# Kernel tuning notes

Measured on AMD Instinct MI355X. Metric: run time of the kernel, lower is better.

## Reference

```python
import jax, jax.numpy as jnp
import numpy as np
import math

SENT_DIM = 1024
HIDDEN_DIM = 1024
NUM_HEADS = 8
ALIGN_DIM = HIDDEN_DIM // NUM_HEADS  # 128
N_SENT = 4096
N_KNOW = 4096


def setup_inputs() -> dict:
    key = jax.random.key(0)
    ks = jax.random.split(key, 12)
    sentences = jax.random.normal(ks[0], (N_SENT, SENT_DIM), dtype=jnp.float32)
    knowledge = jax.random.normal(ks[1], (N_KNOW, SENT_DIM), dtype=jnp.float32)
    # binary multiplicative mask over knowledge entries, broadcast over sentence rows
    mask = (jax.random.uniform(ks[2], (N_KNOW,)) > 0.5).astype(jnp.float32)
    lim_p = 1.0 / math.sqrt(SENT_DIM)
    # per-head projections, stacked: [H, sent_dim, align_dim]
    Ws = jax.random.uniform(ks[3], (NUM_HEADS, SENT_DIM, ALIGN_DIM), minval=-lim_p, maxval=lim_p)
    bs = jax.random.uniform(ks[4], (NUM_HEADS, ALIGN_DIM), minval=-lim_p, maxval=lim_p)
    Wk = jax.random.uniform(ks[5], (NUM_HEADS, SENT_DIM, ALIGN_DIM), minval=-lim_p, maxval=lim_p)
    bk = jax.random.uniform(ks[6], (NUM_HEADS, ALIGN_DIM), minval=-lim_p, maxval=lim_p)
    # transform MLP: Linear(H*sent_dim -> sent_dim), ReLU, (dropout=identity in eval), Linear(sent_dim -> sent_dim)
    lim1 = 1.0 / math.sqrt(NUM_HEADS * SENT_DIM)
    W1 = jax.random.uniform(ks[7], (NUM_HEADS * SENT_DIM, SENT_DIM), minval=-lim1, maxval=lim1)
    b1 = jax.random.uniform(ks[8], (SENT_DIM,), minval=-lim1, maxval=lim1)
    lim2 = 1.0 / math.sqrt(SENT_DIM)
    W2 = jax.random.uniform(ks[9], (SENT_DIM, SENT_DIM), minval=-lim2, maxval=lim2)
    b2 = jax.random.uniform(ks[10], (SENT_DIM,), minval=-lim2, maxval=lim2)
    return {"sentences": sentences, "knowledge": knowledge, "mask": mask,
            "Ws": Ws, "bs": bs, "Wk": Wk, "bk": bk,
            "W1": W1, "b1": b1, "W2": W2, "b2": b2}


def reference(sentences, knowledge, mask, Ws, bs, Wk, bk, W1, b1, W2, b2):
    # Batched over heads (original loops in Python over heads)
    S = jnp.einsum('nd,hde->hne', sentences, Ws) + bs[:, None, :]   # [H, Ns, A]
    K = jnp.einsum('md,hde->hme', knowledge, Wk) + bk[:, None, :]   # [H, Nk, A]
    scores = jnp.einsum('hne,hme->hnm', S, K) / jnp.sqrt(jnp.float32(ALIGN_DIM))
    attn = jax.nn.softmax(scores, axis=-1)                          # softmax over knowledge dim
    attn = attn * mask[None, None, :]                               # post-softmax multiplicative mask
    head_out = jnp.einsum('hnm,md->hnd', attn, knowledge)           # [H, Ns, sent_dim]
    # concat heads along feature dim: [Ns, H*sent_dim]
    concat = jnp.transpose(head_out, (1, 0, 2)).reshape(head_out.shape[1], -1)
    h = jax.nn.relu(concat @ W1 + b1)                               # dropout identity in eval
    output = h @ W2 + b2                                            # [Ns, sent_dim]
    # weights cat along dim 0: [H*Ns, Nk]
    weights = attn.reshape(-1, attn.shape[-1])
    return output, weights
```

## Files before the change

### kernel.cpp

```cpp
#include <hip/hip_runtime.h>
#include <hip/hip_bf16.h>

typedef __attribute__((ext_vector_type(4))) float  floatx4;
typedef __attribute__((ext_vector_type(8))) short  shortx8;
typedef __attribute__((ext_vector_type(4))) short  shortx4;

__device__ __forceinline__ short f2bf(float x) {
    union { float f; unsigned u; } v; v.f = x;
    unsigned r = v.u + 0x7FFFu + ((v.u >> 16) & 1u);
    return (short)(r >> 16);
}
__device__ __forceinline__ float bf2f(short x) {
    union { unsigned u; float f; } c; c.u = ((unsigned)(unsigned short)x) << 16;
    return c.f;
}
__device__ __forceinline__ short f2bf_hw(float x) {
    union { __hip_bfloat16 h; short s; } u;
    u.h = __float2bfloat16(x);
    return u.s;
}

__device__ __forceinline__ void gload16(const void* g, void* l) {
    __builtin_amdgcn_global_load_lds(
        (const __attribute__((address_space(1))) void*)g,
        (__attribute__((address_space(3))) void*)l, 16, 0, 0);
}


__global__ void cast_bf16(const float* __restrict__ src, short* __restrict__ dst, int n4) {
    int i = blockIdx.x * blockDim.x + threadIdx.x;
    if (i < n4) {
        floatx4 v = ((const floatx4*)src)[i];
        shortx4 s;
        s[0] = f2bf(v[0]); s[1] = f2bf(v[1]); s[2] = f2bf(v[2]); s[3] = f2bf(v[3]);
        ((shortx4*)dst)[i] = s;
    }
}

__global__ void transpose_cast(const float* __restrict__ src, short* __restrict__ dst,
                               int R, int C, long szSrc, long szDst) {
    __shared__ float tile[32][33];
    const float* s = src + (long)blockIdx.z * szSrc;
    short* d = dst + (long)blockIdx.z * szDst;
    int c0 = blockIdx.x * 32, r0 = blockIdx.y * 32;
    for (int i = threadIdx.y; i < 32; i += 8)
        tile[i][threadIdx.x] = s[(long)(r0 + i) * C + c0 + threadIdx.x];
    __syncthreads();
    for (int i = threadIdx.y; i < 32; i += 8)
        d[(long)(c0 + i) * R + r0 + threadIdx.x] = f2bf(tile[threadIdx.x][i]);
}


#define BM 128
#define BN 128
#define BK 32

template<bool AF32, bool RELU, bool CF32, bool XSWZ>
__global__ __launch_bounds__(256) void gemm_nt(
    const void* __restrict__ Ap, const short* __restrict__ Bp, void* __restrict__ Cp,
    const float* __restrict__ bias, float alpha,
    int K, int lda, int ldb, int ldc,
    long sAz, long sBz, long sCz, long aHX, long sbias)
{
    __shared__ __align__(16) char  AsB[AF32 ? BM * BK * 4 : BM * BK * 2];
    __shared__ __align__(16) short Bs[BN * BK];
    short* AsS = reinterpret_cast<short*>(AsB);
    float* AsF = reinterpret_cast<float*>(AsB);

    int bx, by, bz;
    if constexpr (XSWZ) {
        int id = blockIdx.x + (blockIdx.y << 3) + (blockIdx.z << 8);
        bx = (id >> 3) & 7;
        int g = (id & 7) | ((id >> 6) << 3);
        by = g & 31; bz = g >> 5;
    } else { bx = blockIdx.x; by = blockIdx.y; bz = blockIdx.z; }

    const int t    = threadIdx.x;
    const int m0   = by * BM;
    const int n0   = bx * BN;
    const int z    = bz;
    const int wave = t >> 6, lane = t & 63;
    const int wm   = (wave & 1) * 64, wn = (wave >> 1) * 64;
    const int quad = lane >> 4, l16 = lane & 15;
    const int wofs = t & ~63;

    const short* Bz = Bp + (long)z * sBz;

    const int srow = t >> 2;
    const int ssw  = ((t & 3) ^ ((t >> 3) & 3)) * 8;
    const short* bSrc = Bz + (long)(n0 + srow) * ldb + ssw;

    const short* aSrc  = nullptr;
    const float* aSrcF = nullptr;
    if constexpr (AF32) {
        const float* Az = (const float*)Ap + (long)z * sAz;
        aSrcF = Az + (long)(m0 + (t >> 3)) * lda + (((t & 7) ^ ((t >> 3) & 7)) * 4);
    } else {
        const short* Az = (const short*)Ap + (long)z * sAz;
        aSrc = Az + (long)(m0 + srow) * lda + ssw;
    }

    const int ra = wm + l16, rb = wn + l16;
    const int sa = (quad ^ ((ra >> 1) & 3)) * 8;
    const int sb = (quad ^ ((rb >> 1) & 3)) * 8;
    const int s0 = (((quad << 1)    ) ^ (ra & 7)) * 4;
    const int s1 = (((quad << 1) | 1) ^ (ra & 7)) * 4;

    floatx4 acc[4][4] = {};

    for (int k0 = 0; k0 < K; k0 += BK) {
        const long off = (long)k0 + (long)(k0 >> 12) * aHX;
        __syncthreads();
        if constexpr (AF32) {
            #pragma unroll
            for (int p = 0; p < 4; ++p)
                gload16(aSrcF + (long)p * 32 * lda + off,
                        AsF + (p * 256 + wofs) * 4);
        } else {
            gload16(aSrc + off,                  AsS + wofs * 8);
            gload16(aSrc + (long)64 * lda + off, AsS + (256 + wofs) * 8);
        }
        gload16(bSrc + k0,                  &Bs[wofs * 8]);
        gload16(bSrc + (long)64 * ldb + k0, &Bs[(256 + wofs) * 8]);
        __syncthreads();

        shortx8 af[4], bfr[4];
        #pragma unroll
        for (int i = 0; i < 4; ++i) {
            if constexpr (AF32) {
                const float* pf = AsF + (ra + 16 * i) * 32;
                floatx4 f0 = *(const floatx4*)(pf + s0);
                floatx4 f1 = *(const floatx4*)(pf + s1);
                shortx8 s;
                s[0] = f2bf_hw(f0[0]); s[1] = f2bf_hw(f0[1]);
                s[2] = f2bf_hw(f0[2]); s[3] = f2bf_hw(f0[3]);
                s[4] = f2bf_hw(f1[0]); s[5] = f2bf_hw(f1[1]);
                s[6] = f2bf_hw(f1[2]); s[7] = f2bf_hw(f1[3]);
                af[i] = s;
            } else {
                af[i] = *(const shortx8*)(AsS + (ra + 16 * i) * 32 + sa);
            }
        }
        #pragma unroll
        for (int j = 0; j < 4; ++j)
            bfr[j] = *(const shortx8*)(&Bs[(rb + 16 * j) * 32 + sb]);
        #pragma unroll
        for (int i = 0; i < 4; ++i)
            #pragma unroll
            for (int j = 0; j < 4; ++j)
                acc[i][j] = __builtin_amdgcn_mfma_f32_16x16x32_bf16(af[i], bfr[j], acc[i][j], 0, 0, 0);
    }

    float bv[4];
    #pragma unroll
    for (int j = 0; j < 4; ++j)
        bv[j] = bias ? (bias + (long)z * sbias)[n0 + wn + j * 16 + l16] : 0.0f;

    #pragma unroll
    for (int i = 0; i < 4; ++i) {
        #pragma unroll
        for (int e = 0; e < 4; ++e) {
            long row = m0 + wm + i * 16 + quad * 4 + e;
            #pragma unroll
            for (int j = 0; j < 4; ++j) {
                float val = acc[i][j][e] * alpha + bv[j];
                if (RELU) val = fmaxf(val, 0.0f);
                long col = n0 + wn + j * 16 + l16;
                if (CF32) ((float*)Cp + (long)z * sCz)[row * ldc + col] = val;
                else      ((short*)Cp + (long)z * sCz)[row * ldc + col] = f2bf(val);
            }
        }
    }
}


__global__ __launch_bounds__(256) void softmax_mask(float* __restrict__ attn,
                                                    const float* __restrict__ mask) {
    float* p = attn + (long)blockIdx.x * 4096;
    const int t = threadIdx.x;
    float v[16];
    float mx = -3.4e38f;
    #pragma unroll
    for (int i = 0; i < 16; ++i) { v[i] = p[t + 256 * i]; mx = fmaxf(mx, v[i]); }
    #pragma unroll
    for (int o = 32; o > 0; o >>= 1) mx = fmaxf(mx, __shfl_down(mx, o));
    __shared__ float r1[4], r2[4];
    const int lane = t & 63, w = t >> 6;
    if (lane == 0) r1[w] = mx;
    __syncthreads();
    mx = fmaxf(fmaxf(r1[0], r1[1]), fmaxf(r1[2], r1[3]));
    float s = 0.f;
    #pragma unroll
    for (int i = 0; i < 16; ++i) { v[i] = __expf(v[i] - mx); s += v[i]; }
    #pragma unroll
    for (int o = 32; o > 0; o >>= 1) s += __shfl_down(s, o);
    if (lane == 0) r2[w] = s;
    __syncthreads();
    s = r2[0] + r2[1] + r2[2] + r2[3];
    const float inv = 1.0f / s;
    #pragma unroll
    for (int i = 0; i < 16; ++i) p[t + 256 * i] = v[i] * inv * mask[t + 256 * i];
}


__global__ __launch_bounds__(256) void reduce_heads(const short* __restrict__ part,
                                                    const float* __restrict__ b1,
                                                    short* __restrict__ h_bf) {
    int i = blockIdx.x * blockDim.x + threadIdx.x;
    float s[8] = {0,0,0,0,0,0,0,0};
    #pragma unroll
    for (int z = 0; z < 4; ++z) {
        shortx8 v = ((const shortx8*)(part + (long)z * 4194304))[i];
        #pragma unroll
        for (int e = 0; e < 8; ++e) s[e] += bf2f(v[e]);
    }
    int j0 = (i * 8) & 1023;
    shortx8 o;
    #pragma unroll
    for (int e = 0; e < 8; ++e) o[e] = f2bf(fmaxf(s[e] + b1[j0 + e], 0.f));
    ((shortx8*)h_bf)[i] = o;
}


extern "C" void kernel_launch(void* const* d_in, const int* in_sizes, int n_in,
                              void* d_out, int out_size, void* d_ws, size_t ws_size,
                              hipStream_t stream) {
    const float* sentences = (const float*)d_in[0];
    const float* knowledge = (const float*)d_in[1];
    const float* mask      = (const float*)d_in[2];
    const float* Ws        = (const float*)d_in[3];
    const float* bs        = (const float*)d_in[4];
    const float* Wk        = (const float*)d_in[5];
    const float* bk        = (const float*)d_in[6];
    const float* W1        = (const float*)d_in[7];
    const float* b1        = (const float*)d_in[8];
    const float* W2        = (const float*)d_in[9];
    const float* b2        = (const float*)d_in[10];

    float* out  = (float*)d_out;
    float* attn = out + 4194304;

    char* ws = (char*)d_ws;
    short* V_T     = (short*)(ws);
    short* W2T     = (short*)(ws + 67108864);
    short* h_bf    = (short*)(ws + 69206016);
    float* bias2   = (float*)(ws + 77594624);
    short* sent_bf = (short*)(ws + 77611008);
    short* know_bf = (short*)(ws + 85999616);
    short* WsT     = (short*)(ws + 94388224);
    short* WkT     = (short*)(ws + 96485376);
    short* W1T     = (short*)(ws + 98582528);
    short* S_bf    = (short*)(ws + 115359744);
    short* K_bf    = (short*)(ws + 123748352);
    short* part    = (short*)(ws + 77611008);
    (void)K_bf;

    cast_bf16<<<4096, 256, 0, stream>>>(sentences, sent_bf, 1048576);
    cast_bf16<<<4096, 256, 0, stream>>>(knowledge, know_bf, 1048576);
    transpose_cast<<<dim3(4, 32, 8),  dim3(32, 8), 0, stream>>>(Ws, WsT, 1024, 128, 131072, 131072);
    transpose_cast<<<dim3(4, 32, 8),  dim3(32, 8), 0, stream>>>(Wk, WkT, 1024, 128, 131072, 131072);
    transpose_cast<<<dim3(32, 32, 8), dim3(32, 8), 0, stream>>>(W1, W1T, 1024, 1024, 1048576, 1048576);
    transpose_cast<<<dim3(32, 32, 1), dim3(32, 8), 0, stream>>>(W2, W2T, 1024, 1024, 0, 0);
    hipMemcpyAsync(bias2,        bs, 4096, hipMemcpyDeviceToDevice, stream);
    hipMemcpyAsync(bias2 + 1024, bk, 4096, hipMemcpyDeviceToDevice, stream);

    gemm_nt<false, false, false, false><<<dim3(8, 32, 2), 256, 0, stream>>>(
        sent_bf, WsT, S_bf, bias2, 1.0f, 1024, 1024, 1024, 1024,
        4194304, 1048576, 4194304, 0, 1024);
    gemm_nt<false, false, false, false><<<dim3(32, 8, 8), 256, 0, stream>>>(
        W1T, know_bf, V_T, nullptr, 1.0f, 1024, 1024, 1024, 32768,
        1048576, 0, 4096, 0, 0);
    gemm_nt<false, false, true, false><<<dim3(32, 32, 8), 256, 0, stream>>>(
        S_bf, K_bf, attn, nullptr, 0.08838834764831845f, 128, 1024, 1024, 4096,
        128, 128, 16777216, 0, 0);
    softmax_mask<<<32768, 256, 0, stream>>>(attn, mask);
    gemm_nt<true, false, false, true><<<dim3(8, 32, 4), 256, 0, stream>>>(
        attn, V_T, part, nullptr, 1.0f, 8192, 4096, 32768, 1024,
        33554432, 8192, 4194304, 16777216 - 4096, 0);
    reduce_heads<<<2048, 256, 0, stream>>>(part, b1, h_bf);
    gemm_nt<false, false, true, false><<<dim3(8, 32, 1), 256, 0, stream>>>(
        h_bf, W2T, out, b2, 1.0f, 1024, 1024, 1024, 1024, 0, 0, 0, 0, 0);
}
```

Baseline: 1.605 ms.

## Double-buffer GEMM LDS tiles and vectorize softmax loads/stores

The GEMM kernel now keeps two LDS buffers and issues the global-to-LDS loads for the next K tile before running the MFMAs on the current tile. This overlaps memory latency with compute and drops one barrier per iteration. The cost is twice the LDS per block, which may lower occupancy, most of all for the fp32-A variant. Separately, the softmax kernel switches to float4 vector loads and stores for the scores and the mask.

```diff
diff --git a/kernel.cpp b/kernel.cpp
--- a/kernel.cpp
+++ b/kernel.cpp
@@ -62,10 +62,9 @@
     int K, int lda, int ldb, int ldc,
     long sAz, long sBz, long sCz, long aHX, long sbias)
 {
-    __shared__ __align__(16) char  AsB[AF32 ? BM * BK * 4 : BM * BK * 2];
-    __shared__ __align__(16) short Bs[BN * BK];
-    short* AsS = reinterpret_cast<short*>(AsB);
-    float* AsF = reinterpret_cast<float*>(AsB);
+    constexpr int ABYTES = AF32 ? (BM * BK * 4) : (BM * BK * 2);
+    __shared__ __align__(16) char  AsB[2 * ABYTES];
+    __shared__ __align__(16) short Bs[2 * BN * BK];
 
     int bx, by, bz;
     if constexpr (XSWZ) {
@@ -106,49 +105,71 @@
     const int s0 = (((quad << 1)    ) ^ (ra & 7)) * 4;
     const int s1 = (((quad << 1) | 1) ^ (ra & 7)) * 4;
 
-    floatx4 acc[4][4] = {};
-
-    for (int k0 = 0; k0 < K; k0 += BK) {
-        const long off = (long)k0 + (long)(k0 >> 12) * aHX;
-        __syncthreads();
+    auto stage = [&](int buf, int kk) {
+        const long off = (long)kk + (long)(kk >> 12) * aHX;
         if constexpr (AF32) {
+            float* ad = (float*)(AsB + buf * ABYTES);
             #pragma unroll
             for (int p = 0; p < 4; ++p)
-                gload16(aSrcF + (long)p * 32 * lda + off,
-                        AsF + (p * 256 + wofs) * 4);
+                gload16(aSrcF + (long)p * 32 * lda + off, ad + (p * 256 + wofs) * 4);
         } else {
-            gload16(aSrc + off,                  AsS + wofs * 8);
-            gload16(aSrc + (long)64 * lda + off, AsS + (256 + wofs) * 8);
+            short* ad = (short*)(AsB + buf * ABYTES);
+            gload16(aSrc + off,                 ad + wofs * 8);
+            gload16(aSrc + (long)64 * lda + off, ad + (256 + wofs) * 8);
         }
-        gload16(bSrc + k0,                  &Bs[wofs * 8]);
-        gload16(bSrc + (long)64 * ldb + k0, &Bs[(256 + wofs) * 8]);
-        __syncthreads();
+        short* bd = Bs + buf * (BN * BK);
+        gload16(bSrc + kk,                  bd + wofs * 8);
+        gload16(bSrc + (long)64 * ldb + kk, bd + (256 + wofs) * 8);
+    };
+
+    floatx4 acc[4][4] = {};
+
+    stage(0, 0);
+    __syncthreads();
+
+    const int nt = K / BK;
+    for (int tt = 0; tt < nt; ++tt) {
+        const int cur = tt & 1;
+        const short* AsS = (const short*)(AsB + cur * ABYTES);
+        const float* AsF = (const float*)(AsB + cur * ABYTES);
+        const short* BsC = Bs + cur * (BN * BK);
 
         shortx8 af[4], bfr[4];
+        floatx4 fa[4][2];
         #pragma unroll
         for (int i = 0; i < 4; ++i) {
             if constexpr (AF32) {
                 const float* pf = AsF + (ra + 16 * i) * 32;
-                floatx4 f0 = *(const floatx4*)(pf + s0);
-                floatx4 f1 = *(const floatx4*)(pf + s1);
-                shortx8 s;
-                s[0] = f2bf_hw(f0[0]); s[1] = f2bf_hw(f0[1]);
-                s[2] = f2bf_hw(f0[2]); s[3] = f2bf_hw(f0[3]);
-                s[4] = f2bf_hw(f1[0]); s[5] = f2bf_hw(f1[1]);
-                s[6] = f2bf_hw(f1[2]); s[7] = f2bf_hw(f1[3]);
-                af[i] = s;
+                fa[i][0] = *(const floatx4*)(pf + s0);
+                fa[i][1] = *(const floatx4*)(pf + s1);
             } else {
                 af[i] = *(const shortx8*)(AsS + (ra + 16 * i) * 32 + sa);
             }
         }
         #pragma unroll
         for (int j = 0; j < 4; ++j)
-            bfr[j] = *(const shortx8*)(&Bs[(rb + 16 * j) * 32 + sb]);
+            bfr[j] = *(const shortx8*)(BsC + (rb + 16 * j) * 32 + sb);
+
+        if (tt + 1 < nt) stage(cur ^ 1, (tt + 1) * BK);
+
+        if constexpr (AF32) {
+            #pragma unroll
+            for (int i = 0; i < 4; ++i) {
+                shortx8 s;
+                s[0] = f2bf_hw(fa[i][0][0]); s[1] = f2bf_hw(fa[i][0][1]);
+                s[2] = f2bf_hw(fa[i][0][2]); s[3] = f2bf_hw(fa[i][0][3]);
+                s[4] = f2bf_hw(fa[i][1][0]); s[5] = f2bf_hw(fa[i][1][1]);
+                s[6] = f2bf_hw(fa[i][1][2]); s[7] = f2bf_hw(fa[i][1][3]);
+                af[i] = s;
+            }
+        }
         #pragma unroll
         for (int i = 0; i < 4; ++i)
             #pragma unroll
             for (int j = 0; j < 4; ++j)
                 acc[i][j] = __builtin_amdgcn_mfma_f32_16x16x32_bf16(af[i], bfr[j], acc[i][j], 0, 0, 0);
+
+        __syncthreads();
     }
 
     float bv[4];
@@ -178,10 +199,13 @@
                                                     const float* __restrict__ mask) {
     float* p = attn + (long)blockIdx.x * 4096;
     const int t = threadIdx.x;
-    float v[16];
+    floatx4 v[4];
     float mx = -3.4e38f;
     #pragma unroll
-    for (int i = 0; i < 16; ++i) { v[i] = p[t + 256 * i]; mx = fmaxf(mx, v[i]); }
+    for (int i = 0; i < 4; ++i) {
+        v[i] = ((const floatx4*)p)[t + 256 * i];
+        mx = fmaxf(mx, fmaxf(fmaxf(v[i][0], v[i][1]), fmaxf(v[i][2], v[i][3])));
+    }
     #pragma unroll
     for (int o = 32; o > 0; o >>= 1) mx = fmaxf(mx, __shfl_down(mx, o));
     __shared__ float r1[4], r2[4];
@@ -191,7 +215,10 @@
     mx = fmaxf(fmaxf(r1[0], r1[1]), fmaxf(r1[2], r1[3]));
     float s = 0.f;
     #pragma unroll
-    for (int i = 0; i < 16; ++i) { v[i] = __expf(v[i] - mx); s += v[i]; }
+    for (int i = 0; i < 4; ++i) {
+        #pragma unroll
+        for (int e = 0; e < 4; ++e) { v[i][e] = __expf(v[i][e] - mx); s += v[i][e]; }
+    }
     #pragma unroll
     for (int o = 32; o > 0; o >>= 1) s += __shfl_down(s, o);
     if (lane == 0) r2[w] = s;
@@ -199,7 +226,13 @@
     s = r2[0] + r2[1] + r2[2] + r2[3];
     const float inv = 1.0f / s;
     #pragma unroll
-    for (int i = 0; i < 16; ++i) p[t + 256 * i] = v[i] * inv * mask[t + 256 * i];
+    for (int i = 0; i < 4; ++i) {
+        floatx4 mv = ((const floatx4*)mask)[t + 256 * i];
+        floatx4 o;
+        #pragma unroll
+        for (int e = 0; e < 4; ++e) o[e] = v[i][e] * inv * mv[e];
+        ((floatx4*)p)[t + 256 * i] = o;
+    }
 }
 
 
```

New measurement: 1.548 ms. 1.04x faster.
